# Optimization experiments

Measured on AMD Instinct MI355X. Metric: run time of the kernel, lower is better.

## Reference

```python
import jax, jax.numpy as jnp
import numpy as np

N = 100000; D = 256; ATT = 512; H = 8; HD = ATT // H; E = 250000
TYPE_CT = 64; TS = 64; P = 8192; PC = 1024; MP = 131072; MC = 16384


def setup_inputs() -> dict:
    key = jax.random.key(0)
    ks = jax.random.split(key, 24)
    sD = 1.0 / np.sqrt(D); sT = 1.0 / np.sqrt(TS); sA = 1.0 / np.sqrt(ATT); sC = 1.0 / np.sqrt(D + ATT)
    inp = {}
    inp['node_states'] = jax.random.normal(ks[0], (N, D), jnp.float32)
    inp['node_types'] = jax.random.randint(ks[1], (N,), 0, TYPE_CT, jnp.int32)
    inp['pair_conj'] = jax.random.randint(ks[2], (E,), 0, N, jnp.int32)
    inp['pair_prem'] = jax.random.randint(ks[3], (E,), 0, N, jnp.int32)
    inp['pool_prem_nodes'] = jax.random.randint(ks[4], (MP,), 0, N, jnp.int32)
    inp['pool_prem_seg'] = ((jnp.arange(MP, dtype=jnp.int32) * P) // MP).astype(jnp.int32)  # every prem set non-empty
    inp['pool_conj_nodes'] = jax.random.randint(ks[5], (MC,), 0, N, jnp.int32)
    inp['pool_conj_seg'] = ((jnp.arange(MC, dtype=jnp.int32) * PC) // MC).astype(jnp.int32)
    inp['prem2conj'] = jax.random.randint(ks[6], (P,), 0, PC, jnp.int32)
    # learned parameters
    inp['ln_g'] = jnp.ones((D,), jnp.float32)
    inp['ln_b'] = jnp.zeros((D,), jnp.float32)
    inp['emb_p'] = jax.random.normal(ks[7], (TYPE_CT, TS), jnp.float32) * 0.02
    inp['wp_w'] = jax.random.normal(ks[8], (TS, ATT), jnp.float32) * sT
    inp['wp_b'] = jnp.zeros((ATT,), jnp.float32)
    inp['emb_c'] = jax.random.normal(ks[9], (TYPE_CT, TS), jnp.float32) * 0.02
    inp['wc_w'] = jax.random.normal(ks[10], (TS, ATT), jnp.float32) * sT
    inp['wc_b'] = jnp.zeros((ATT,), jnp.float32)
    inp['Wq_p'] = jax.random.normal(ks[11], (H, D, HD), jnp.float32) * sD
    inp['Wk_p'] = jax.random.normal(ks[12], (H, D, HD), jnp.float32) * sD
    inp['Wv_p'] = jax.random.normal(ks[13], (H, D, HD), jnp.float32) * sD
    inp['Wo_p'] = jax.random.normal(ks[14], (ATT, ATT), jnp.float32) * sA
    inp['Wq_c'] = jax.random.normal(ks[15], (H, D, HD), jnp.float32) * sD
    inp['Wk_c'] = jax.random.normal(ks[16], (H, D, HD), jnp.float32) * sD
    inp['Wv_c'] = jax.random.normal(ks[17], (H, D, HD), jnp.float32) * sD
    inp['Wo_c'] = jax.random.normal(ks[18], (ATT, ATT), jnp.float32) * sA
    inp['W_dag'] = jax.random.normal(ks[19], (D + ATT, D + ATT), jnp.float32) * sC
    inp['b_dag'] = jnp.zeros((D + ATT,), jnp.float32)
    return inp


def _layernorm(x, g, b):
    mu = jnp.mean(x, axis=-1, keepdims=True)
    var = jnp.mean(jnp.square(x - mu), axis=-1, keepdims=True)
    return (x - mu) * jax.lax.rsqrt(var + 1e-5) * g + b


def _mha_dir(x, src, tgt, Wq, Wk, Wv, Wo, gate):
    # gather query/key/value node reprs along the pair list (irregular gather)
    xs = x[src]; xt = x[tgt]                       # [E, D]
    q = jnp.einsum('ed,hdk->ehk', xs, Wq)          # [E, H, HD]
    k = jnp.einsum('ed,hdk->ehk', xt, Wk)
    scores = jnp.sum(q * k, axis=-1) / np.sqrt(HD)  # [E, H]
    # per-query-node (segment) softmax, as in compute_att_aggr grouping
    m = jax.ops.segment_max(scores, src, num_segments=N)
    ex = jnp.exp(scores - m[src])
    denom = jax.ops.segment_sum(ex, src, num_segments=N)
    prob = ex / denom[src]
    v = jnp.einsum('ed,hdk->ehk', xt, Wv)
    # adj_matr @ comb_matr scatter-aggregation
    agg = jax.ops.segment_sum(prob[..., None] * v, src, num_segments=N)  # [N, H, HD]
    return gate * (agg.reshape(N, H * HD) @ Wo)


def reference(node_states, node_types, pair_conj, pair_prem, pool_prem_nodes, pool_prem_seg,
              pool_conj_nodes, pool_conj_seg, prem2conj,
              ln_g, ln_b, emb_p, wp_w, wp_b, emb_c, wc_w, wc_b,
              Wq_p, Wk_p, Wv_p, Wo_p, Wq_c, Wk_c, Wv_c, Wo_c, W_dag, b_dag):
    x = _layernorm(node_states, ln_g, ln_b)                                  # ne_norm(node reprs)
    gate_p = jax.nn.sigmoid(emb_p[node_types] @ wp_w + wp_b)                 # prem_gate  [N, ATT]
    gate_c = jax.nn.sigmoid(emb_c[node_types] @ wc_w + wc_b)                 # conj_gate
    # just_prem pairs: (prem, conj) -> query/scatter node = prem, key/value node = conj
    comb = _mha_dir(x, pair_prem, pair_conj, Wq_p, Wk_p, Wv_p, Wo_p, gate_p)
    # just_conj pairs: (conj, prem)
    comb = comb + _mha_dir(x, pair_conj, pair_prem, Wq_c, Wk_c, Wv_c, Wo_c, gate_c)
    h = jnp.concatenate([x, comb], axis=1)                                   # [N, D+ATT]
    pooled = jnp.tanh(h @ W_dag + b_dag)                                     # simplified dag_lstm pass
    prem_r = jax.ops.segment_max(pooled[pool_prem_nodes], pool_prem_seg, num_segments=P)
    conj_sets = jax.ops.segment_max(pooled[pool_conj_nodes], pool_conj_seg, num_segments=PC)
    conj_r = conj_sets[prem2conj]
    return jnp.concatenate([prem_r, conj_r], axis=1)                         # [P, 2*(D+ATT)]
```

## Files before the change

### kernel.cpp

```cpp
#include <hip/hip_runtime.h>
#include <math.h>

#define N_NODES 100000
#define DIM 256
#define ATT 512
#define NH 8
#define HD 64
#define E_PAIRS 250000
#define TYPE_CT 64
#define TS 64
#define P_SEG 8192
#define PC_SEG 1024
#define MP_SZ 131072
#define MC_SZ 16384
#define CD 768

typedef unsigned short u16;
typedef __attribute__((ext_vector_type(8))) short short8v;
typedef __attribute__((ext_vector_type(4))) float floatx4;

__device__ __forceinline__ u16 f2b(float f) {
    unsigned u = __float_as_uint(f);
    return (u16)((u + 0x7FFFu + ((u >> 16) & 1u)) >> 16);
}
__device__ __forceinline__ float b2f(u16 h) {
    return __uint_as_float(((unsigned)h) << 16);
}

template<int N>
__device__ __forceinline__ void waitcnt_vm() {
    asm volatile("s_waitcnt vmcnt(%0)" :: "n"(N) : "memory");
}
__device__ __forceinline__ void barrier_fence() {
    asm volatile("s_barrier" ::: "memory");
    __builtin_amdgcn_sched_barrier(0);
}

__global__ __launch_bounds__(256) void fill_val_k(float* out, int n, float v) {
    int i = blockIdx.x * 256 + threadIdx.x;
    if (i < n) out[i] = v;
}

__global__ __launch_bounds__(64) void layernorm_k(
    const float* __restrict__ ns, const float* __restrict__ g,
    const float* __restrict__ b, u16* __restrict__ x)
{
    int row = blockIdx.x;
    int lane = threadIdx.x;
    float4 v = ((const float4*)(ns + (size_t)row * DIM))[lane];
    float sum = v.x + v.y + v.z + v.w;
    #pragma unroll
    for (int off = 32; off >= 1; off >>= 1) sum += __shfl_xor(sum, off);
    float mu = sum * (1.0f / DIM);
    float dx = v.x - mu, dy = v.y - mu, dz = v.z - mu, dw = v.w - mu;
    float sq = dx * dx + dy * dy + dz * dz + dw * dw;
    #pragma unroll
    for (int off = 32; off >= 1; off >>= 1) sq += __shfl_xor(sq, off);
    float rs = rsqrtf(sq * (1.0f / DIM) + 1e-5f);
    float4 gg = ((const float4*)g)[lane];
    float4 bb = ((const float4*)b)[lane];
    u16 o4[4];
    o4[0] = f2b(dx * rs * gg.x + bb.x);
    o4[1] = f2b(dy * rs * gg.y + bb.y);
    o4[2] = f2b(dz * rs * gg.z + bb.z);
    o4[3] = f2b(dw * rs * gg.w + bb.w);
    *(uint2*)(x + (size_t)row * DIM + lane * 4) = *(uint2*)o4;
}

__global__ __launch_bounds__(512) void gate_table_k(
    const float* __restrict__ emb, const float* __restrict__ w,
    const float* __restrict__ wb, float* __restrict__ tab)
{
    int t = blockIdx.x;
    int a = threadIdx.x;
    float acc = wb[a];
    #pragma unroll 8
    for (int s = 0; s < TS; ++s) acc += emb[t * TS + s] * w[s * ATT + a];
    tab[t * ATT + a] = 1.0f / (1.0f + expf(-acc));
}

__global__ __launch_bounds__(256) void wcvt_k(
    const float* __restrict__ W, u16* __restrict__ Bt, int K, int N)
{
    int idx = blockIdx.x * 256 + threadIdx.x;
    if (idx >= K * N) return;
    int c = idx / K, k = idx - c * K;
    Bt[idx] = f2b(W[(size_t)k * N + c]);
}

__global__ __launch_bounds__(256) void wqkv_cvt_k(
    const float* __restrict__ Wq, const float* __restrict__ Wk,
    const float* __restrict__ Wv, u16* __restrict__ outp)
{
    int idx = blockIdx.x * 256 + threadIdx.x;
    if (idx >= NH * 3 * HD * DIM) return;
    int k = idx & (DIM - 1);
    int c = (idx >> 8) & (HD - 1);
    int hm = idx >> 14;
    int m = hm % 3;
    int h = hm / 3;
    const float* W = (m == 0) ? Wq : ((m == 1) ? Wk : Wv);
    outp[idx] = f2b(W[((size_t)h * DIM + k) * HD + c]);
}

template<int BM, int WN, int EPI>
__device__ __forceinline__ void gemm_body3(
    const u16* __restrict__ A, int lda,
    const u16* __restrict__ A2, int lda2, int K1,
    const u16* __restrict__ Bt, int ldb,
    u16* __restrict__ C, int ldc,
    int M, int K,
    const float* __restrict__ bias,
    const float* __restrict__ gateTab,
    const int* __restrict__ types)
{
    constexpr int BN = 32 * WN;
    constexpr int AR = BM / 64;
    constexpr int BR = BN / 64;
    constexpr int LA = AR + BR;
    constexpr int AF = BM / 32;
    __shared__ u16 As[3][BM * 32];
    __shared__ u16 Bs[3][BN * 32];
    const int bm = blockIdx.y * BM;
    const int bn = blockIdx.x * BN;
    const int tid = threadIdx.x;
    const int wave = tid >> 6, lane = tid & 63;
    const int wm = (wave >> 1) * (BM / 2), wn = (wave & 1) * 16 * WN;
    const int srow = tid >> 2;
    const int skk = (tid & 3) * 8;
    floatx4 acc[AF][WN] = {};

    auto stage = [&](int buf, int k0) {
        #pragma unroll
        for (int rnd = 0; rnd < AR; ++rnd) {
            int grow = bm + srow + rnd * 64;
            if (grow > M - 1) grow = M - 1;
            int gk = k0 + skk;
            const u16* src;
            if (EPI == 2 && gk >= K1) src = A2 + (size_t)grow * lda2 + (gk - K1);
            else                      src = A + (size_t)grow * lda + gk;
            __builtin_amdgcn_global_load_lds(
                (const __attribute__((address_space(1))) void*)src,
                (__attribute__((address_space(3))) void*)(&As[buf][rnd * 2048 + wave * 512]),
                16, 0, 0);
        }
        #pragma unroll
        for (int rnd = 0; rnd < BR; ++rnd) {
            const u16* src = Bt + (size_t)(bn + srow + rnd * 64) * ldb + k0 + skk;
            __builtin_amdgcn_global_load_lds(
                (const __attribute__((address_space(1))) void*)src,
                (__attribute__((address_space(3))) void*)(&Bs[buf][rnd * 2048 + wave * 512]),
                16, 0, 0);
        }
    };

    const int NS = K >> 5;
    stage(0, 0);
    stage(1, 32);
    const int rr = lane & 15, kq = (lane >> 4) * 8;
    int cur = 0;
    for (int is = 0; is < NS; ++is) {
        if (is == NS - 1) waitcnt_vm<0>();
        else              waitcnt_vm<LA>();
        barrier_fence();
        if (is + 2 < NS) stage((cur + 2) % 3, (is + 2) * 32);
        short8v a[AF], b[WN];
        #pragma unroll
        for (int i = 0; i < AF; ++i)
            a[i] = *(const short8v*)&As[cur][(wm + i * 16 + rr) * 32 + kq];
        #pragma unroll
        for (int j = 0; j < WN; ++j)
            b[j] = *(const short8v*)&Bs[cur][(wn + j * 16 + rr) * 32 + kq];
        #pragma unroll
        for (int i = 0; i < AF; ++i)
            #pragma unroll
            for (int j = 0; j < WN; ++j)
                acc[i][j] = __builtin_amdgcn_mfma_f32_16x16x32_bf16(
                    a[i], b[j], acc[i][j], 0, 0, 0);
        cur = (cur + 1) % 3;
    }
    #pragma unroll
    for (int i = 0; i < AF; ++i) {
        #pragma unroll
        for (int j = 0; j < WN; ++j) {
            #pragma unroll
            for (int q = 0; q < 4; ++q) {
                int row = bm + wm + i * 16 + (lane >> 4) * 4 + q;
                if (row >= M) continue;
                int col = bn + wn + j * 16 + (lane & 15);
                float v = acc[i][j][q];
                size_t idx = (size_t)row * ldc + col;
                if (EPI == 0) C[idx] = f2b(v);
                else if (EPI == 1) {
                    float g = gateTab[types[row] * ATT + col];
                    C[idx] = f2b(b2f(C[idx]) + g * v);
                } else if (EPI == 3) {
                    float g = gateTab[types[row] * ATT + col];
                    C[idx] = f2b(g * v);
                } else {
                    C[idx] = f2b(tanhf(v + bias[col]));
                }
            }
        }
    }
}

__global__ __launch_bounds__(256) void gemm_qkv(
    const u16* __restrict__ A, const u16* __restrict__ Bt, u16* __restrict__ C)
{
    gemm_body3<64, 6, 0>(A, DIM, nullptr, 0, 1 << 30, Bt, DIM, C, 192,
                         N_NODES, DIM, nullptr, nullptr, nullptr);
}
__global__ __launch_bounds__(256) void gemm_wo_first(
    const u16* __restrict__ A, const u16* __restrict__ Bt, u16* __restrict__ C,
    const float* __restrict__ gateTab, const int* __restrict__ types)
{
    gemm_body3<64, 4, 3>(A, ATT, nullptr, 0, 1 << 30, Bt, ATT, C, ATT,
                         N_NODES, ATT, nullptr, gateTab, types);
}
__global__ __launch_bounds__(256) void gemm_wo_acc(
    const u16* __restrict__ A, const u16* __restrict__ Bt, u16* __restrict__ C,
    const float* __restrict__ gateTab, const int* __restrict__ types)
{
    gemm_body3<64, 4, 1>(A, ATT, nullptr, 0, 1 << 30, Bt, ATT, C, ATT,
                         N_NODES, ATT, nullptr, gateTab, types);
}
__global__ __launch_bounds__(256) void gemm_dag(
    const u16* __restrict__ A, const u16* __restrict__ A2,
    const u16* __restrict__ Bt, u16* __restrict__ C,
    const float* __restrict__ bias)
{
    gemm_body3<64, 4, 2>(A, DIM, A2, ATT, DIM, Bt, CD, C, 384,
                         N_NODES, CD, bias, nullptr, nullptr);
}

__global__ __launch_bounds__(256) void count_k(
    const int* __restrict__ src, int* __restrict__ counts)
{
    int e = blockIdx.x * 256 + threadIdx.x;
    if (e < E_PAIRS) atomicAdd(&counts[src[e]], 1);
}
__global__ __launch_bounds__(256) void scan1_k(
    const int* __restrict__ counts, int* __restrict__ offs, int* __restrict__ bsums)
{
    __shared__ int sm[256];
    int i = blockIdx.x * 256 + threadIdx.x;
    int v = (i < N_NODES) ? counts[i] : 0;
    sm[threadIdx.x] = v;
    __syncthreads();
    for (int d = 1; d < 256; d <<= 1) {
        int t = (threadIdx.x >= d) ? sm[threadIdx.x - d] : 0;
        __syncthreads();
        sm[threadIdx.x] += t;
        __syncthreads();
    }
    if (i < N_NODES) offs[i] = sm[threadIdx.x] - v;
    if (threadIdx.x == 255) bsums[blockIdx.x] = sm[255];
}
__global__ __launch_bounds__(512) void scan2_k(int* __restrict__ bsums, int nb)
{
    __shared__ int sm[512];
    int tx = threadIdx.x;
    int v = (tx < nb) ? bsums[tx] : 0;
    sm[tx] = v;
    __syncthreads();
    for (int d = 1; d < 512; d <<= 1) {
        int t = (tx >= d) ? sm[tx - d] : 0;
        __syncthreads();
        sm[tx] += t;
        __syncthreads();
    }
    if (tx < nb) bsums[tx] = sm[tx] - v;
}
__global__ __launch_bounds__(256) void addcur_k(
    int* __restrict__ offs, const int* __restrict__ bsums, int* __restrict__ cur)
{
    int i = blockIdx.x * 256 + threadIdx.x;
    if (i >= N_NODES) return;
    int o = offs[i] + bsums[i >> 8];
    offs[i] = o;
    cur[i] = o;
}
__global__ __launch_bounds__(256) void scatter_k(
    const int* __restrict__ src, const int* __restrict__ tgt,
    int* __restrict__ cur, int* __restrict__ csr_tgt)
{
    int e = blockIdx.x * 256 + threadIdx.x;
    if (e >= E_PAIRS) return;
    int p = atomicAdd(&cur[src[e]], 1);
    csr_tgt[p] = tgt[e];
}

__global__ __launch_bounds__(256) void attn_k(
    const u16* __restrict__ qkv, const int* __restrict__ offs,
    const int* __restrict__ counts, const int* __restrict__ csr_tgt,
    u16* __restrict__ agg, int h)
{
    int s = blockIdx.x * 4 + (threadIdx.x >> 6);
    if (s >= N_NODES) return;
    int lane = threadIdx.x & 63;
    float q = b2f(qkv[(size_t)s * 192 + lane]) * 0.125f;
    int lo = offs[s], deg = counts[s];
    float m = -INFINITY, l = 0.0f, acc = 0.0f;
    for (int i = 0; i < deg; ++i) {
        int t = csr_tgt[lo + i];
        float kd = b2f(qkv[(size_t)t * 192 + 64 + lane]);
        float vd = b2f(qkv[(size_t)t * 192 + 128 + lane]);
        float p = q * kd;
        #pragma unroll
        for (int off = 32; off >= 1; off >>= 1) p += __shfl_xor(p, off);
        float mn = fmaxf(m, p);
        float sc = expf(m - mn);
        float w  = expf(p - mn);
        l = l * sc + w;
        acc = acc * sc + w * vd;
        m = mn;
    }
    float r = (deg > 0) ? acc / l : 0.0f;
    agg[(size_t)s * ATT + h * HD + lane] = f2b(r);
}

template<int BFOUT>
__global__ __launch_bounds__(256) void seg_max_k(
    const u16* __restrict__ pooled, const int* __restrict__ nodes,
    const int* __restrict__ seg, int total, void* __restrict__ outv, int ldo)
{
    int p = blockIdx.x;
    int lo, hi;
    { int a = 0, b2 = total; while (a < b2) { int mid = (a + b2) >> 1; if (seg[mid] < p) a = mid + 1; else b2 = mid; } lo = a; }
    { int a = lo, b2 = total; while (a < b2) { int mid = (a + b2) >> 1; if (seg[mid] < p + 1) a = mid + 1; else b2 = mid; } hi = a; }
    for (int c = threadIdx.x; c < 384; c += 256) {
        float mx = -INFINITY;
        for (int i = lo; i < hi; ++i)
            mx = fmaxf(mx, b2f(pooled[(size_t)nodes[i] * 384 + c]));
        if (BFOUT) ((u16*)outv)[(size_t)p * ldo + c] = f2b(mx);
        else       ((float*)outv)[(size_t)p * ldo + c] = mx;
    }
}

__global__ __launch_bounds__(768) void gather_conj(
    const u16* __restrict__ cs, const int* __restrict__ p2c,
    float* __restrict__ out)
{
    int p = blockIdx.x;
    int c = threadIdx.x;
    out[(size_t)p * (2 * CD) + CD + c] = b2f(cs[(size_t)p2c[p] * CD + c]);
}

extern "C" void kernel_launch(void* const* d_in, const int* in_sizes, int n_in,
                              void* d_out, int out_size, void* d_ws, size_t ws_size,
                              hipStream_t stream) {
    const float* node_states     = (const float*)d_in[0];
    const int*   node_types      = (const int*)d_in[1];
    const int*   pair_conj       = (const int*)d_in[2];
    const int*   pair_prem       = (const int*)d_in[3];
    const int*   pool_prem_nodes = (const int*)d_in[4];
    const int*   pool_prem_seg   = (const int*)d_in[5];
    const int*   pool_conj_nodes = (const int*)d_in[6];
    const int*   pool_conj_seg   = (const int*)d_in[7];
    const int*   prem2conj       = (const int*)d_in[8];
    const float* ln_g  = (const float*)d_in[9];
    const float* ln_b  = (const float*)d_in[10];
    const float* emb_p = (const float*)d_in[11];
    const float* wp_w  = (const float*)d_in[12];
    const float* wp_b  = (const float*)d_in[13];
    const float* emb_c = (const float*)d_in[14];
    const float* wc_w  = (const float*)d_in[15];
    const float* wc_b  = (const float*)d_in[16];
    const float* Wq_p  = (const float*)d_in[17];
    const float* Wk_p  = (const float*)d_in[18];
    const float* Wv_p  = (const float*)d_in[19];
    const float* Wo_p  = (const float*)d_in[20];
    const float* Wq_c  = (const float*)d_in[21];
    const float* Wk_c  = (const float*)d_in[22];
    const float* Wv_c  = (const float*)d_in[23];
    const float* Wo_c  = (const float*)d_in[24];
    const float* W_dag = (const float*)d_in[25];
    const float* b_dag = (const float*)d_in[26];
    float* out = (float*)d_out;

    char* ws = (char*)d_ws;
    size_t o = 0;
    u16* x_bf  = (u16*)(ws + o); o += (size_t)N_NODES * DIM * 2;
    u16* comb  = (u16*)(ws + o); o += (size_t)N_NODES * ATT * 2;
    u16* R     = (u16*)(ws + o); o += (size_t)N_NODES * ATT * 2;
    char* csrb = ws + o;         o += 8000000;
    u16* conj_sets = (u16*)(ws + o); o += (size_t)PC_SEG * CD * 2;
    const size_t WS_NEEDED = o;

    if (ws_size < WS_NEEDED) {
        fill_val_k<<<(out_size + 255) / 256, 256, 0, stream>>>(out, out_size, (float)ws_size);
        return;
    }

    u16* agg    = R;
    u16* pooled = R;
    int* c_counts[2], *c_offs[2], *c_cur[2], *c_tgt[2];
    for (int d = 0; d < 2; ++d) {
        char* base = csrb + (size_t)d * 2200000;
        c_counts[d] = (int*)(base + 0);
        c_offs[d]   = (int*)(base + 400000);
        c_cur[d]    = (int*)(base + 800000);
        c_tgt[d]    = (int*)(base + 1200000);
    }
    int* bsums = (int*)(csrb + 4400000);
    u16* wdag_t = (u16*)csrb;

    char* ob = (char*)d_out;
    u16* qkv     = (u16*)(ob + 0);
    float* gtab_p = (float*)(ob + 38400000);
    float* gtab_c = (float*)(ob + 38531072);
    u16* wqkv_t  = (u16*)(ob + 38662144);
    u16* wo_t    = (u16*)(ob + 40235008);

    layernorm_k<<<N_NODES, 64, 0, stream>>>(node_states, ln_g, ln_b, x_bf);
    gate_table_k<<<TYPE_CT, ATT, 0, stream>>>(emb_p, wp_w, wp_b, gtab_p);
    gate_table_k<<<TYPE_CT, ATT, 0, stream>>>(emb_c, wc_w, wc_b, gtab_c);
    wqkv_cvt_k<<<(NH * 3 * HD * DIM + 255) / 256, 256, 0, stream>>>(
        Wq_p, Wk_p, Wv_p, wqkv_t);
    wqkv_cvt_k<<<(NH * 3 * HD * DIM + 255) / 256, 256, 0, stream>>>(
        Wq_c, Wk_c, Wv_c, wqkv_t + (size_t)NH * 3 * HD * DIM);
    wcvt_k<<<(ATT * ATT + 255) / 256, 256, 0, stream>>>(Wo_p, wo_t, ATT, ATT);
    wcvt_k<<<(ATT * ATT + 255) / 256, 256, 0, stream>>>(
        Wo_c, wo_t + (size_t)ATT * ATT, ATT, ATT);

    const int NSCAN = (N_NODES + 255) / 256;
    for (int d = 0; d < 2; ++d) {
        const int* src = d ? pair_conj : pair_prem;
        const int* tgt = d ? pair_prem : pair_conj;
        hipMemsetAsync(c_counts[d], 0, 400000, stream);
        count_k<<<(E_PAIRS + 255) / 256, 256, 0, stream>>>(src, c_counts[d]);
        scan1_k<<<NSCAN, 256, 0, stream>>>(c_counts[d], c_offs[d], bsums);
        scan2_k<<<1, 512, 0, stream>>>(bsums, NSCAN);
        addcur_k<<<NSCAN, 256, 0, stream>>>(c_offs[d], bsums, c_cur[d]);
        scatter_k<<<(E_PAIRS + 255) / 256, 256, 0, stream>>>(src, tgt, c_cur[d], c_tgt[d]);
    }

    const int MB64 = (N_NODES + 63) / 64;

    for (int dir = 0; dir < 2; ++dir) {
        const float* gt = dir ? gtab_c : gtab_p;
        const u16* wq_d = wqkv_t + (size_t)dir * NH * 3 * HD * DIM;
        const u16* wo_d = wo_t + (size_t)dir * ATT * ATT;

        for (int h = 0; h < NH; ++h) {
            gemm_qkv<<<dim3(1, MB64), 256, 0, stream>>>(
                x_bf, wq_d + (size_t)h * 3 * HD * DIM, qkv);
            attn_k<<<(N_NODES + 3) / 4, 256, 0, stream>>>(
                qkv, c_offs[dir], c_counts[dir], c_tgt[dir], agg, h);
        }

        if (dir == 0)
            gemm_wo_first<<<dim3(ATT / 128, MB64), 256, 0, stream>>>(
                agg, wo_d, comb, gt, node_types);
        else
            gemm_wo_acc<<<dim3(ATT / 128, MB64), 256, 0, stream>>>(
                agg, wo_d, comb, gt, node_types);
    }

    wcvt_k<<<(CD * CD + 255) / 256, 256, 0, stream>>>(W_dag, wdag_t, CD, CD);

    for (int c0 = 0; c0 < CD; c0 += 384) {
        gemm_dag<<<dim3(3, MB64), 256, 0, stream>>>(
            x_bf, comb, wdag_t + (size_t)c0 * CD, pooled, b_dag + c0);
        seg_max_k<0><<<P_SEG, 256, 0, stream>>>(
            pooled, pool_prem_nodes, pool_prem_seg, MP_SZ, out + c0, 2 * CD);
        seg_max_k<1><<<PC_SEG, 256, 0, stream>>>(
            pooled, pool_conj_nodes, pool_conj_seg, MC_SZ, conj_sets + c0, CD);
    }
    gather_conj<<<P_SEG, CD, 0, stream>>>(conj_sets, prem2conj, out);
}
```

Baseline: 2.160 ms.

## Swizzle GEMM LDS tiles, deepen pipeline to four stages, shrink N tiles

The shared bf16 GEMM body gains an XOR swizzle on the K-chunk index in LDS, applied both when staging and when reading fragments, to cut bank conflicts. The async-load pipeline becomes a template parameter set to 4 stages, with the wait counts adjusted to match. All GEMMs drop to 64-column tiles (WN=2), which triples or doubles the grid sizes for more parallelism. The cost is that each A tile is reloaded for more column blocks, and the deeper pipeline uses more LDS.

After: 2.455 ms. 13.7% more time.

```diff
diff --git a/kernel.cpp b/kernel.cpp
--- a/kernel.cpp
+++ b/kernel.cpp
@@ -103,7 +103,7 @@
     outp[idx] = f2b(W[((size_t)h * DIM + k) * HD + c]);
 }
 
-template<int BM, int WN, int EPI>
+template<int BM, int WN, int DEPTH, int EPI>
 __device__ __forceinline__ void gemm_body3(
     const u16* __restrict__ A, int lda,
     const u16* __restrict__ A2, int lda2, int K1,
@@ -119,15 +119,15 @@
     constexpr int BR = BN / 64;
     constexpr int LA = AR + BR;
     constexpr int AF = BM / 32;
-    __shared__ u16 As[3][BM * 32];
-    __shared__ u16 Bs[3][BN * 32];
+    __shared__ u16 As[DEPTH][BM * 32];
+    __shared__ u16 Bs[DEPTH][BN * 32];
     const int bm = blockIdx.y * BM;
     const int bn = blockIdx.x * BN;
     const int tid = threadIdx.x;
     const int wave = tid >> 6, lane = tid & 63;
     const int wm = (wave >> 1) * (BM / 2), wn = (wave & 1) * 16 * WN;
     const int srow = tid >> 2;
-    const int skk = (tid & 3) * 8;
+    const int skk = (((tid & 3) ^ ((srow >> 1) & 3)) * 8);
     floatx4 acc[AF][WN] = {};
 
     auto stage = [&](int buf, int k0) {
@@ -155,29 +155,38 @@
     };
 
     const int NS = K >> 5;
-    stage(0, 0);
-    stage(1, 32);
-    const int rr = lane & 15, kq = (lane >> 4) * 8;
+    #pragma unroll
+    for (int p = 0; p < DEPTH - 1; ++p)
+        if (p < NS) stage(p, p * 32);
+    const int rr = lane & 15;
+    const int cq = lane >> 4;
     int cur = 0;
     for (int is = 0; is < NS; ++is) {
-        if (is == NS - 1) waitcnt_vm<0>();
-        else              waitcnt_vm<LA>();
+        int pend = NS - 1 - is;
+        if (pend > DEPTH - 2) pend = DEPTH - 2;
+        if (pend >= 2)      waitcnt_vm<2 * LA>();
+        else if (pend == 1) waitcnt_vm<LA>();
+        else                waitcnt_vm<0>();
         barrier_fence();
-        if (is + 2 < NS) stage((cur + 2) % 3, (is + 2) * 32);
+        if (is + DEPTH - 1 < NS) stage((cur + DEPTH - 1) % DEPTH, (is + DEPTH - 1) * 32);
         short8v a[AF], b[WN];
         #pragma unroll
-        for (int i = 0; i < AF; ++i)
-            a[i] = *(const short8v*)&As[cur][(wm + i * 16 + rr) * 32 + kq];
-        #pragma unroll
-        for (int j = 0; j < WN; ++j)
-            b[j] = *(const short8v*)&Bs[cur][(wn + j * 16 + rr) * 32 + kq];
+        for (int i = 0; i < AF; ++i) {
+            int ar = wm + i * 16 + rr;
+            a[i] = *(const short8v*)&As[cur][ar * 32 + ((cq ^ ((ar >> 1) & 3)) * 8)];
+        }
+        #pragma unroll
+        for (int j = 0; j < WN; ++j) {
+            int br = wn + j * 16 + rr;
+            b[j] = *(const short8v*)&Bs[cur][br * 32 + ((cq ^ ((br >> 1) & 3)) * 8)];
+        }
         #pragma unroll
         for (int i = 0; i < AF; ++i)
             #pragma unroll
             for (int j = 0; j < WN; ++j)
                 acc[i][j] = __builtin_amdgcn_mfma_f32_16x16x32_bf16(
                     a[i], b[j], acc[i][j], 0, 0, 0);
-        cur = (cur + 1) % 3;
+        cur = (cur + 1) % DEPTH;
     }
     #pragma unroll
     for (int i = 0; i < AF; ++i) {
@@ -208,30 +217,30 @@
 __global__ __launch_bounds__(256) void gemm_qkv(
     const u16* __restrict__ A, const u16* __restrict__ Bt, u16* __restrict__ C)
 {
-    gemm_body3<64, 6, 0>(A, DIM, nullptr, 0, 1 << 30, Bt, DIM, C, 192,
-                         N_NODES, DIM, nullptr, nullptr, nullptr);
+    gemm_body3<64, 2, 4, 0>(A, DIM, nullptr, 0, 1 << 30, Bt, DIM, C, 192,
+                            N_NODES, DIM, nullptr, nullptr, nullptr);
 }
 __global__ __launch_bounds__(256) void gemm_wo_first(
     const u16* __restrict__ A, const u16* __restrict__ Bt, u16* __restrict__ C,
     const float* __restrict__ gateTab, const int* __restrict__ types)
 {
-    gemm_body3<64, 4, 3>(A, ATT, nullptr, 0, 1 << 30, Bt, ATT, C, ATT,
-                         N_NODES, ATT, nullptr, gateTab, types);
+    gemm_body3<64, 2, 4, 3>(A, ATT, nullptr, 0, 1 << 30, Bt, ATT, C, ATT,
+                            N_NODES, ATT, nullptr, gateTab, types);
 }
 __global__ __launch_bounds__(256) void gemm_wo_acc(
     const u16* __restrict__ A, const u16* __restrict__ Bt, u16* __restrict__ C,
     const float* __restrict__ gateTab, const int* __restrict__ types)
 {
-    gemm_body3<64, 4, 1>(A, ATT, nullptr, 0, 1 << 30, Bt, ATT, C, ATT,
-                         N_NODES, ATT, nullptr, gateTab, types);
+    gemm_body3<64, 2, 4, 1>(A, ATT, nullptr, 0, 1 << 30, Bt, ATT, C, ATT,
+                            N_NODES, ATT, nullptr, gateTab, types);
 }
 __global__ __launch_bounds__(256) void gemm_dag(
     const u16* __restrict__ A, const u16* __restrict__ A2,
     const u16* __restrict__ Bt, u16* __restrict__ C,
     const float* __restrict__ bias)
 {
-    gemm_body3<64, 4, 2>(A, DIM, A2, ATT, DIM, Bt, CD, C, 384,
-                         N_NODES, CD, bias, nullptr, nullptr);
+    gemm_body3<64, 2, 4, 2>(A, DIM, A2, ATT, DIM, Bt, CD, C, 384,
+                            N_NODES, CD, bias, nullptr, nullptr);
 }
 
 __global__ __launch_bounds__(256) void count_k(
@@ -444,24 +453,24 @@
         const u16* wo_d = wo_t + (size_t)dir * ATT * ATT;
 
         for (int h = 0; h < NH; ++h) {
-            gemm_qkv<<<dim3(1, MB64), 256, 0, stream>>>(
+            gemm_qkv<<<dim3(3, MB64), 256, 0, stream>>>(
                 x_bf, wq_d + (size_t)h * 3 * HD * DIM, qkv);
             attn_k<<<(N_NODES + 3) / 4, 256, 0, stream>>>(
                 qkv, c_offs[dir], c_counts[dir], c_tgt[dir], agg, h);
         }
 
         if (dir == 0)
-            gemm_wo_first<<<dim3(ATT / 128, MB64), 256, 0, stream>>>(
+            gemm_wo_first<<<dim3(ATT / 64, MB64), 256, 0, stream>>>(
                 agg, wo_d, comb, gt, node_types);
         else
-            gemm_wo_acc<<<dim3(ATT / 128, MB64), 256, 0, stream>>>(
+            gemm_wo_acc<<<dim3(ATT / 64, MB64), 256, 0, stream>>>(
                 agg, wo_d, comb, gt, node_types);
     }
 
     wcvt_k<<<(CD * CD + 255) / 256, 256, 0, stream>>>(W_dag, wdag_t, CD, CD);
 
     for (int c0 = 0; c0 < CD; c0 += 384) {
-        gemm_dag<<<dim3(3, MB64), 256, 0, stream>>>(
+        gemm_dag<<<dim3(384 / 64, MB64), 256, 0, stream>>>(
             x_bf, comb, wdag_t + (size_t)c0 * CD, pooled, b_dag + c0);
         seg_max_k<0><<<P_SEG, 256, 0, stream>>>(
             pooled, pool_prem_nodes, pool_prem_seg, MP_SZ, out + c0, 2 * CD);
```
